# Performance work log

Measured on AMD Instinct MI355X. Metric: run time of the kernel, lower is better.

The kernel has to match this reference:

```python
import jax, jax.numpy as jnp
import numpy as np

D_MODEL = 16   # output feature dim of channel_proj
D_STATE = 8
D_CONV = 2
D_INNER = 4    # expand * inner mamba d_model (2*2)
DT_RANK = 1    # ceil(2/16)
NUM_PAIRS = 36
B, W, T = 8, 8, 1024


def setup_inputs() -> dict:
    key = jax.random.key(0)
    ks = jax.random.split(key, 12)
    s = 0.5
    return {
        "raw_signals": jax.random.normal(ks[0], (B, W, NUM_PAIRS, 2, T), jnp.float32),
        "in_proj_w": jax.random.normal(ks[1], (2 * D_INNER, 2), jnp.float32) * s,
        "conv_w": jax.random.normal(ks[2], (D_INNER, D_CONV), jnp.float32) * s,
        "conv_b": jax.random.normal(ks[3], (D_INNER,), jnp.float32) * 0.1,
        "x_proj_w": jax.random.normal(ks[4], (DT_RANK + 2 * D_STATE, D_INNER), jnp.float32) * s,
        "dt_proj_w": jax.random.normal(ks[5], (D_INNER, DT_RANK), jnp.float32) * s,
        "dt_proj_b": jax.random.normal(ks[6], (D_INNER,), jnp.float32) * 0.1,
        # S4D-real init: A_log = log(arange(1..d_state)) per inner channel
        "A_log": jnp.log(jnp.broadcast_to(jnp.arange(1, D_STATE + 1, dtype=jnp.float32), (D_INNER, D_STATE))),
        "D_skip": jnp.ones((D_INNER,), jnp.float32),
        "out_proj_w": jax.random.normal(ks[7], (2, D_INNER), jnp.float32) * s,
        "proj_w": jax.random.normal(ks[8], (D_MODEL, 2), jnp.float32) * s,
        "proj_b": jax.random.normal(ks[9], (D_MODEL,), jnp.float32) * 0.1,
    }


def _mamba_forward(x_in, in_proj_w, conv_w, conv_b, x_proj_w, dt_proj_w,
                   dt_proj_b, A_log, D_skip, out_proj_w):
    # x_in: (N, T, 2)
    N, Tlen, _ = x_in.shape
    xz = jnp.einsum('ntc,dc->ntd', x_in, in_proj_w)          # (N,T,2*d_inner)
    x, z = jnp.split(xz, 2, axis=-1)                          # (N,T,d_inner) each
    # causal depthwise conv1d, kernel size D_CONV
    xp = jnp.pad(x, ((0, 0), (D_CONV - 1, 0), (0, 0)))
    x = sum(xp[:, k:k + Tlen] * conv_w[:, k] for k in range(D_CONV)) + conv_b
    x = jax.nn.silu(x)
    # input-dependent dt, B, C
    x_dbl = jnp.einsum('ntd,ed->nte', x, x_proj_w)            # (N,T,dt_rank+2*d_state)
    dt, Bm, Cm = jnp.split(x_dbl, [DT_RANK, DT_RANK + D_STATE], axis=-1)
    dt = jax.nn.softplus(jnp.einsum('ntr,dr->ntd', dt, dt_proj_w) + dt_proj_b)
    A = -jnp.exp(A_log)                                       # (d_inner,d_state)
    deltaA = jnp.exp(dt[..., None] * A)                       # (N,T,d_inner,d_state)
    deltaBx = dt[..., None] * Bm[:, :, None, :] * x[..., None]

    def step(h, inputs):
        dA_t, dBx_t, c_t = inputs
        h = dA_t * h + dBx_t                                  # (N,d_inner,d_state)
        y_t = jnp.einsum('nds,ns->nd', h, c_t)
        return h, y_t

    h0 = jnp.zeros((N, D_INNER, D_STATE), x.dtype)
    _, ys = jax.lax.scan(
        step, h0,
        (deltaA.transpose(1, 0, 2, 3), deltaBx.transpose(1, 0, 2, 3), Cm.transpose(1, 0, 2)))
    y = ys.transpose(1, 0, 2) + x * D_skip                    # (N,T,d_inner)
    y = y * jax.nn.silu(z)
    return jnp.einsum('ntd,cd->ntc', y, out_proj_w)           # (N,T,2)


def reference(raw_signals, in_proj_w, conv_w, conv_b, x_proj_w, dt_proj_w,
              dt_proj_b, A_log, D_skip, out_proj_w, proj_w, proj_b):
    Bsz, Wn, P, C, Tlen = raw_signals.shape
    # per-window loop in torch does identical math -> flatten windows into batch
    x_in = raw_signals.transpose(0, 1, 2, 4, 3).reshape(-1, Tlen, C)  # (B*W*P, T, 2)
    out = _mamba_forward(x_in, in_proj_w, conv_w, conv_b, x_proj_w, dt_proj_w,
                         dt_proj_b, A_log, D_skip, out_proj_w)
    feat = out.mean(axis=1)                                   # (B*W*P, 2)
    proj = jax.nn.relu(feat @ proj_w.T + proj_b)              # dropout is eval no-op
    proj = proj.reshape(Bsz, Wn, P, -1)                       # (B,W,P,d_model)
    return proj.mean(axis=2)                                  # (B,W,d_model)
```

## Files before the change

### kernel.cpp

```cpp
#include <hip/hip_runtime.h>
#include <hip/hip_fp16.h>


typedef float v2f __attribute__((ext_vector_type(2)));

#define TT 1024
#define TC 32
#define NSEGS 8
#define SEGLEN (TT / NSEGS)
#define NCHUNK (SEGLEN / TC)
#define NUM_PAIRS 36
#define NSEQ 2304

#define DT_OFF 0
#define DS_OFF 128
#define BC_OFF 256
#define BC_STRIDE 33
#define PER_HALF_STRIDE 528
#define PER_WAVE (2 * PER_HALF_STRIDE)
#define STAGE_TOTAL (4 * PER_WAVE)

__device__ __forceinline__ float fast_silu(float v) {
    float e = __builtin_amdgcn_exp2f(v * -1.4426950408889634f);
    return v * __builtin_amdgcn_rcpf(1.0f + e);
}
__device__ __forceinline__ float fast_softplus(float v) {
    float e = __builtin_amdgcn_exp2f(v * 1.4426950408889634f);
    return __builtin_amdgcn_logf(1.0f + e) * 0.6931471805599453f;
}
__device__ __forceinline__ uint pk_h2(float a, float b) {
    return __builtin_bit_cast(uint, __builtin_amdgcn_cvt_pkrtz(a, b));
}

__global__ __launch_bounds__(256, 4)
void pm_kernel(const float* __restrict__ raw,
               const float* __restrict__ in_proj_w,
               const float* __restrict__ conv_w,
               const float* __restrict__ conv_b,
               const float* __restrict__ x_proj_w,
               const float* __restrict__ dt_proj_w,
               const float* __restrict__ dt_proj_b,
               const float* __restrict__ A_log,
               const float* __restrict__ D_skip,
               const float* __restrict__ out_proj_w,
               const float* __restrict__ proj_w,
               const float* __restrict__ proj_b,
               float* __restrict__ out)
{
    __shared__ float lds[STAGE_TOTAL];

    const int tid  = threadIdx.x;
    const int wid  = tid >> 6;
    const int lane = tid & 63;
    const int half = lane >> 5;
    const int lh   = lane & 31;
    const int g    = wid * 2 + half;
    const int n    = blockIdx.x;
    const float* rp = raw + (size_t)n * (2 * TT);

    float* hb = lds + wid * PER_WAVE + half * PER_HALF_STRIDE;

    float ip0[8], ip1[8];
#pragma unroll
    for (int j = 0; j < 8; ++j) { ip0[j] = in_proj_w[2*j]; ip1[j] = in_proj_w[2*j+1]; }
    float cw0[4], cw1[4], cbv[4], dpw[4], dpb[4], Dsk[4], ow0[4], ow1[4], xp0[4];
#pragma unroll
    for (int d = 0; d < 4; ++d) {
        cw0[d] = conv_w[2*d]; cw1[d] = conv_w[2*d+1]; cbv[d] = conv_b[d];
        dpw[d] = dt_proj_w[d]; dpb[d] = dt_proj_b[d];
        Dsk[d] = D_skip[d]; ow0[d] = out_proj_w[d]; ow1[d] = out_proj_w[4+d];
        xp0[d] = x_proj_w[d];
    }
    v2f xbc[8][4];
#pragma unroll
    for (int s = 0; s < 8; ++s)
#pragma unroll
        for (int d = 0; d < 4; ++d)
            xbc[s][d] = (v2f){x_proj_w[4*(1+s) + d], x_proj_w[4*(9+s) + d]};

    const float LOG2E = 1.4426950408889634f;
    const int   d_idx = lh >> 3;
    const int   s_idx = lh & 7;
    const float A2ds  = -__expf(A_log[lh]) * LOG2E;
    const float owd0  = out_proj_w[d_idx];
    const float owd1  = out_proj_w[4 + d_idx];

    const float* dtp = hb + DT_OFF + d_idx;
    const uint*  dsp = (const uint*)(hb + DS_OFF) + d_idx;
    const uint*  bcp = (const uint*)(hb + BC_OFF) + s_idx * BC_STRIDE;

    float A_run = 1.0f, hB = 0.0f, W = 0.0f, S = 0.0f;
    float sacc0 = 0.f, sacc1 = 0.f;

    const int seg0 = g * SEGLEN;

    int t0 = seg0 + lh;
    float c0  = rp[t0];
    float c1  = rp[TT + t0];
    float c0m = (t0 > 0) ? rp[t0 - 1]      : 0.0f;
    float c1m = (t0 > 0) ? rp[TT + t0 - 1] : 0.0f;

    for (int chunk = 0; chunk < NCHUNK; ++chunk) {
        float p0 = 0.f, p1 = 0.f, p0m = 0.f, p1m = 0.f;
        if (chunk + 1 < NCHUNK) {
            int tn = seg0 + (chunk + 1) * TC + lh;
            p0  = rp[tn];       p1  = rp[TT + tn];
            p0m = rp[tn - 1];   p1m = rp[TT + tn - 1];
        }

        float x[4], sz[4];
#pragma unroll
        for (int d = 0; d < 4; ++d) {
            float xz  = ip0[d]*c0  + ip1[d]*c1;
            float xm1 = ip0[d]*c0m + ip1[d]*c1m;
            float zv  = ip0[4+d]*c0 + ip1[4+d]*c1;
            float v   = xm1*cw0[d] + xz*cw1[d] + cbv[d];
            x[d]  = fast_silu(v);
            sz[d] = fast_silu(zv);
        }

        float dtin = xp0[0]*x[0] + xp0[1]*x[1] + xp0[2]*x[2] + xp0[3]*x[3];

        v2f bc[8];
#pragma unroll
        for (int s = 0; s < 8; ++s) {
            v2f a = xbc[s][0] * (v2f){x[0], x[0]};
            a = __builtin_elementwise_fma(xbc[s][1], (v2f){x[1], x[1]}, a);
            a = __builtin_elementwise_fma(xbc[s][2], (v2f){x[2], x[2]}, a);
            bc[s] = __builtin_elementwise_fma(xbc[s][3], (v2f){x[3], x[3]}, a);
        }

        float dt[4];
#pragma unroll
        for (int d = 0; d < 4; ++d) {
            dt[d] = fast_softplus(dtin*dpw[d] + dpb[d]);
            float g2 = x[d] * Dsk[d] * sz[d];
            sacc0 = fmaf(g2, ow0[d], sacc0);
            sacc1 = fmaf(g2, ow1[d], sacc1);
        }

        *(float4*)(hb + DT_OFF + lh*4) = make_float4(dt[0], dt[1], dt[2], dt[3]);
        *(uint4*)((uint*)(hb + DS_OFF) + lh*4) =
            make_uint4(pk_h2(dt[0]*x[0], sz[0]), pk_h2(dt[1]*x[1], sz[1]),
                       pk_h2(dt[2]*x[2], sz[2]), pk_h2(dt[3]*x[3], sz[3]));
        uint* bcw = (uint*)(hb + BC_OFF) + lh;
#pragma unroll
        for (int s = 0; s < 8; ++s)
            bcw[s * BC_STRIDE] = pk_h2(bc[s].x, bc[s].y);

#pragma unroll
        for (int t2 = 0; t2 < TC; ++t2) {
            float dtv = dtp[t2*4];
            uint  uds = dsp[t2*4];
            uint  ubc = bcp[t2];
            __half2 prod = __hmul2(__builtin_bit_cast(__half2, uds),
                                   __builtin_bit_cast(__half2, ubc));
            float b = __half2float(__low2half(prod));
            float q = __half2float(__high2half(prod));
            float a = __builtin_amdgcn_exp2f(dtv * A2ds);
            A_run *= a;
            hB = fmaf(a, hB, b);
            W  = fmaf(A_run, q, W);
            S  = fmaf(hB, q, S);
        }

        c0 = p0; c1 = p1; c0m = p0m; c1m = p1m;
    }

    __syncthreads();
    float2* comb = (float2*)lds;
    comb[g*32 + lh] = make_float2(A_run, hB);
    __syncthreads();

    float h_in = 0.0f;
#pragma unroll
    for (int gg = 0; gg < NSEGS - 1; ++gg) {
        if (gg < g) {
            float2 abg = comb[gg*32 + lh];
            h_in = fmaf(abg.x, h_in, abg.y);
        }
    }

    float F = fmaf(h_in, W, S);
    float tot0 = fmaf(F, owd0, sacc0);
    float tot1 = fmaf(F, owd1, sacc1);
#pragma unroll
    for (int m = 16; m >= 1; m >>= 1) {
        tot0 += __shfl_xor(tot0, m, 64);
        tot1 += __shfl_xor(tot1, m, 64);
    }
    float* part = lds + 512;
    if (lh == 0) {
        part[g*2]     = tot0;
        part[g*2 + 1] = tot1;
    }
    __syncthreads();

    if (tid < 16) {
        float f0 = 0.f, f1 = 0.f;
#pragma unroll
        for (int gg = 0; gg < NSEGS; ++gg) {
            f0 += part[gg*2];
            f1 += part[gg*2 + 1];
        }
        f0 *= (1.0f / (float)TT);
        f1 *= (1.0f / (float)TT);
        float pv = f0*proj_w[2*tid] + f1*proj_w[2*tid + 1] + proj_b[tid];
        pv = fmaxf(pv, 0.0f);
        atomicAdd(out + (n / NUM_PAIRS) * 16 + tid, pv * (1.0f / NUM_PAIRS));
    }
}

extern "C" void kernel_launch(void* const* d_in, const int* in_sizes, int n_in,
                              void* d_out, int out_size, void* d_ws, size_t ws_size,
                              hipStream_t stream)
{
    const float* raw        = (const float*)d_in[0];
    const float* in_proj_w  = (const float*)d_in[1];
    const float* conv_w     = (const float*)d_in[2];
    const float* conv_b     = (const float*)d_in[3];
    const float* x_proj_w   = (const float*)d_in[4];
    const float* dt_proj_w  = (const float*)d_in[5];
    const float* dt_proj_b  = (const float*)d_in[6];
    const float* A_log      = (const float*)d_in[7];
    const float* D_skip     = (const float*)d_in[8];
    const float* out_proj_w = (const float*)d_in[9];
    const float* proj_w     = (const float*)d_in[10];
    const float* proj_b     = (const float*)d_in[11];

    hipMemsetAsync(d_out, 0, (size_t)out_size * sizeof(float), stream);

    pm_kernel<<<dim3(NSEQ), dim3(256), 0, stream>>>(
        raw, in_proj_w, conv_w, conv_b, x_proj_w, dt_proj_w, dt_proj_b,
        A_log, D_skip, out_proj_w, proj_w, proj_b, (float*)d_out);
}
```

Before: 116.3 us.

## Split each sequence into 16 scan segments with 512-thread blocks; fold conv into in_proj

Doubles the number of time segments per sequence to 16, using 8 waves per block, so each half-wave scans 64 timesteps instead of 128. This shortens the serial recurrence per thread. The cost is a longer cross-segment combine, twice the LDS per block, and possibly lower block residency. It also precomputes conv weights multiplied by in_proj weights and evaluates the conv and z projections as packed v2f FMAs, cutting per-timestep ALU work.

```diff
diff --git a/kernel.cpp b/kernel.cpp
--- a/kernel.cpp
+++ b/kernel.cpp
@@ -6,7 +6,7 @@
 
 #define TT 1024
 #define TC 32
-#define NSEGS 8
+#define NSEGS 16
 #define SEGLEN (TT / NSEGS)
 #define NCHUNK (SEGLEN / TC)
 #define NUM_PAIRS 36
@@ -18,7 +18,7 @@
 #define BC_STRIDE 33
 #define PER_HALF_STRIDE 528
 #define PER_WAVE (2 * PER_HALF_STRIDE)
-#define STAGE_TOTAL (4 * PER_WAVE)
+#define STAGE_TOTAL (8 * PER_WAVE)
 
 __device__ __forceinline__ float fast_silu(float v) {
     float e = __builtin_amdgcn_exp2f(v * -1.4426950408889634f);
@@ -32,7 +32,7 @@
     return __builtin_bit_cast(uint, __builtin_amdgcn_cvt_pkrtz(a, b));
 }
 
-__global__ __launch_bounds__(256, 4)
+__global__ __launch_bounds__(512, 4)
 void pm_kernel(const float* __restrict__ raw,
                const float* __restrict__ in_proj_w,
                const float* __restrict__ conv_w,
@@ -63,13 +63,26 @@
     float ip0[8], ip1[8];
 #pragma unroll
     for (int j = 0; j < 8; ++j) { ip0[j] = in_proj_w[2*j]; ip1[j] = in_proj_w[2*j+1]; }
-    float cw0[4], cw1[4], cbv[4], dpw[4], dpb[4], Dsk[4], ow0[4], ow1[4], xp0[4];
+    float dpw[4], dpb[4], Dsk[4], ow0[4], ow1[4], xp0[4];
+    v2f alp[2], bep[2], gap[2], dep[2], cbp[2], zc0[2], zc1[2];
 #pragma unroll
     for (int d = 0; d < 4; ++d) {
-        cw0[d] = conv_w[2*d]; cw1[d] = conv_w[2*d+1]; cbv[d] = conv_b[d];
         dpw[d] = dt_proj_w[d]; dpb[d] = dt_proj_b[d];
         Dsk[d] = D_skip[d]; ow0[d] = out_proj_w[d]; ow1[d] = out_proj_w[4+d];
         xp0[d] = x_proj_w[d];
+    }
+#pragma unroll
+    for (int k = 0; k < 2; ++k) {
+        int d0 = 2*k, d1 = 2*k + 1;
+        float cw00 = conv_w[2*d0], cw01 = conv_w[2*d0+1];
+        float cw10 = conv_w[2*d1], cw11 = conv_w[2*d1+1];
+        alp[k] = (v2f){cw00*ip0[d0], cw10*ip0[d1]};
+        bep[k] = (v2f){cw00*ip1[d0], cw10*ip1[d1]};
+        gap[k] = (v2f){cw01*ip0[d0], cw11*ip0[d1]};
+        dep[k] = (v2f){cw01*ip1[d0], cw11*ip1[d1]};
+        cbp[k] = (v2f){conv_b[d0], conv_b[d1]};
+        zc0[k] = (v2f){ip0[4+d0], ip0[4+d1]};
+        zc1[k] = (v2f){ip1[4+d0], ip1[4+d1]};
     }
     v2f xbc[8][4];
 #pragma unroll
@@ -109,14 +122,19 @@
         }
 
         float x[4], sz[4];
-#pragma unroll
-        for (int d = 0; d < 4; ++d) {
-            float xz  = ip0[d]*c0  + ip1[d]*c1;
-            float xm1 = ip0[d]*c0m + ip1[d]*c1m;
-            float zv  = ip0[4+d]*c0 + ip1[4+d]*c1;
-            float v   = xm1*cw0[d] + xz*cw1[d] + cbv[d];
-            x[d]  = fast_silu(v);
-            sz[d] = fast_silu(zv);
+        const v2f c0v = {c0, c0}, c1v = {c1, c1};
+        const v2f c0mv = {c0m, c0m}, c1mv = {c1m, c1m};
+#pragma unroll
+        for (int k = 0; k < 2; ++k) {
+            v2f v = __builtin_elementwise_fma(alp[k], c0mv,
+                    __builtin_elementwise_fma(bep[k], c1mv,
+                    __builtin_elementwise_fma(gap[k], c0v,
+                    __builtin_elementwise_fma(dep[k], c1v, cbp[k]))));
+            v2f zv = __builtin_elementwise_fma(zc0[k], c0v, zc1[k] * c1v);
+            x[2*k]    = fast_silu(v.x);
+            x[2*k+1]  = fast_silu(v.y);
+            sz[2*k]   = fast_silu(zv.x);
+            sz[2*k+1] = fast_silu(zv.y);
         }
 
         float dtin = xp0[0]*x[0] + xp0[1]*x[1] + xp0[2]*x[2] + xp0[3]*x[3];
@@ -189,7 +207,7 @@
         tot0 += __shfl_xor(tot0, m, 64);
         tot1 += __shfl_xor(tot1, m, 64);
     }
-    float* part = lds + 512;
+    float* part = lds + 1024;
     if (lh == 0) {
         part[g*2]     = tot0;
         part[g*2 + 1] = tot1;
@@ -230,7 +248,7 @@
 
     hipMemsetAsync(d_out, 0, (size_t)out_size * sizeof(float), stream);
 
-    pm_kernel<<<dim3(NSEQ), dim3(256), 0, stream>>>(
+    pm_kernel<<<dim3(NSEQ), dim3(512), 0, stream>>>(
         raw, in_proj_w, conv_w, conv_b, x_proj_w, dt_proj_w, dt_proj_b,
         A_log, D_skip, out_proj_w, proj_w, proj_b, (float*)d_out);
 }
```

Result: slower. 122.8 us (+5.6%).
